# Performance work log

Measured on AMD Instinct MI355X. Metric: run time of the kernel, lower is better.

## Reference

```python
import jax, jax.numpy as jnp
import numpy as np

N, E, H, C, B = 20000, 320000, 4, 64, 64
D = H * C  # 256, output_dim_gnn
NEG_SLOPE = 0.2
EPS = 1e-5


def setup_inputs() -> dict:
    key = jax.random.key(0)
    ks = iter(jax.random.split(key, 40))
    s = 0.05
    inp = {}
    inp['x'] = jax.random.normal(next(ks), (N, 5), jnp.float32)
    inp['edge_index'] = jax.random.randint(next(ks), (2, E), 0, N, jnp.int64)
    inp['edge_attr'] = jax.random.normal(next(ks), (E, 63), jnp.float32)
    inp['batch'] = jnp.sort(jax.random.randint(next(ks), (N,), 0, B, jnp.int64))
    # node / edge embedding linears
    inp['node_W'] = jax.random.normal(next(ks), (5, D), jnp.float32) * s
    inp['node_b'] = jnp.zeros((D,), jnp.float32)
    inp['edge_W'] = jax.random.normal(next(ks), (63, D), jnp.float32) * s
    inp['edge_b'] = jnp.zeros((D,), jnp.float32)
    # two GATv2 layers + batch norms
    for i in range(2):
        inp[f'Wl{i}'] = jax.random.normal(next(ks), (D, H * C), jnp.float32) * s
        inp[f'bl{i}'] = jnp.zeros((H * C,), jnp.float32)
        inp[f'Wr{i}'] = jax.random.normal(next(ks), (D, H * C), jnp.float32) * s
        inp[f'br{i}'] = jnp.zeros((H * C,), jnp.float32)
        inp[f'We{i}'] = jax.random.normal(next(ks), (D, H * C), jnp.float32) * s
        inp[f'att{i}'] = jax.random.normal(next(ks), (H, C), jnp.float32) * s
        inp[f'bias{i}'] = jnp.zeros((H * C,), jnp.float32)
        inp[f'gamma{i}'] = jnp.ones((D,), jnp.float32)
        inp[f'beta{i}'] = jnp.zeros((D,), jnp.float32)
    # final MLP + output layer
    inp['mlp_W'] = jax.random.normal(next(ks), (D, C), jnp.float32) * s
    inp['mlp_b'] = jnp.zeros((C,), jnp.float32)
    inp['out_W'] = jax.random.normal(next(ks), (C, 5), jnp.float32) * s
    inp['out_b'] = jnp.zeros((5,), jnp.float32)
    return inp


def gatv2_conv(x, src, dst, e, Wl, bl, Wr, br, We, att, bias):
    # x: [N, D]; e: [E, D] (embedded edge features)
    xl = (x @ Wl + bl).reshape(N, H, C)  # source-side transform (lin_l)
    xr = (x @ Wr + br).reshape(N, H, C)  # target-side transform (lin_r)
    ee = (e @ We).reshape(E, H, C)       # lin_edge (no bias in PyG)
    m = xl[src] + xr[dst] + ee           # [E, H, C]
    alpha = jnp.einsum('ehc,hc->eh', jax.nn.leaky_relu(m, NEG_SLOPE), att)
    # segment softmax over incoming edges of each target node
    amax = jax.ops.segment_max(alpha, dst, num_segments=N)[dst]
    ex = jnp.exp(alpha - amax)
    denom = jax.ops.segment_sum(ex, dst, num_segments=N)[dst]
    a = ex / denom                        # [E, H]
    out = jax.ops.segment_sum(xl[src] * a[:, :, None], dst, num_segments=N)
    return out.reshape(N, H * C) + bias


def batch_norm(x, gamma, beta):
    mu = jnp.mean(x, axis=0)
    var = jnp.mean((x - mu) ** 2, axis=0)  # biased var (training-mode norm)
    return (x - mu) * jax.lax.rsqrt(var + EPS) * gamma + beta


def reference(x, edge_index, edge_attr, batch,
              node_W, node_b, edge_W, edge_b,
              Wl0, bl0, Wr0, br0, We0, att0, bias0, gamma0, beta0,
              Wl1, bl1, Wr1, br1, We1, att1, bias1, gamma1, beta1,
              mlp_W, mlp_b, out_W, out_b):
    src, dst = edge_index[0], edge_index[1]
    h = x @ node_W + node_b          # [N, D]
    e = edge_attr @ edge_W + edge_b  # [E, D]
    h = gatv2_conv(h, src, dst, e, Wl0, bl0, Wr0, br0, We0, att0, bias0)
    h = jax.nn.relu(batch_norm(h, gamma0, beta0))
    h = gatv2_conv(h, src, dst, e, Wl1, bl1, Wr1, br1, We1, att1, bias1)
    h = jax.nn.relu(batch_norm(h, gamma1, beta1))
    h = jax.nn.relu(h @ mlp_W + mlp_b)  # [N, C]
    # global mean pool per graph
    pooled = jax.ops.segment_sum(h, batch, num_segments=B)
    cnt = jax.ops.segment_sum(jnp.ones((N,), h.dtype), batch, num_segments=B)
    pooled = pooled / jnp.maximum(cnt, 1.0)[:, None]
    return pooled @ out_W + out_b  # [B, n_classes]
```

## Files before the change

### kernel.cpp

```cpp
#include <hip/hip_runtime.h>

#define NN 20000
#define EE 320000
#define BB 64

typedef _Float16 half8 __attribute__((ext_vector_type(8)));
typedef _Float16 half4 __attribute__((ext_vector_type(4)));
typedef float floatx4 __attribute__((ext_vector_type(4)));

__global__ void k_prep_edgeW(const float* __restrict__ edge_W, const float* __restrict__ edge_b,
                             const float* __restrict__ We0, const float* __restrict__ We1,
                             _Float16* __restrict__ Wpt0, _Float16* __restrict__ Wpt1) {
    __shared__ float row[256];
    int k = blockIdx.x, layer = blockIdx.y, j = threadIdx.x;
    row[j] = (k < 63) ? edge_W[k*256 + j] : edge_b[j];
    __syncthreads();
    const float* We = layer ? We1 : We0;
    float acc = 0.f;
    for (int t = 0; t < 256; ++t) acc += row[t] * We[t*256 + j];
    (layer ? Wpt1 : Wpt0)[j*64 + k] = (_Float16)acc;
}

__global__ void k_prep_acat(const float* __restrict__ node_W, const float* __restrict__ node_b,
                            const float* __restrict__ Wl0, const float* __restrict__ bl0,
                            const float* __restrict__ Wr0, const float* __restrict__ br0,
                            float* __restrict__ Acat) {
    __shared__ float row[256];
    int k = blockIdx.x, j = threadIdx.x;
    if (j < 256) row[j] = (k < 5) ? node_W[k*256 + j] : node_b[j];
    __syncthreads();
    int jj = j & 255;
    const float* W = (j < 256) ? Wl0 : Wr0;
    float acc = 0.f;
    for (int t = 0; t < 256; ++t) acc += row[t] * W[t*256 + jj];
    if (k == 5) acc += (j < 256) ? bl0[jj] : br0[jj];
    Acat[k*512 + j] = acc;
}

__global__ void k_prep_t16(const float* __restrict__ Wl1, const float* __restrict__ bl1,
                           const float* __restrict__ Wr1, const float* __restrict__ br1,
                           const float* __restrict__ mlp_W,
                           _Float16* __restrict__ WlWr1t, float* __restrict__ blr1,
                           _Float16* __restrict__ mlpWt) {
    int n = blockIdx.x, k = threadIdx.x;
    if (n < 512) {
        float v = (n < 256) ? Wl1[k*256 + n] : Wr1[k*256 + (n - 256)];
        WlWr1t[n*256 + k] = (_Float16)v;
        if (k == 0) blr1[n] = (n < 256) ? bl1[n] : br1[n - 256];
    } else {
        int nn = n - 512;
        mlpWt[nn*256 + k] = (_Float16)mlp_W[k*64 + nn];
    }
}

__global__ void k_hist(const int* __restrict__ ei, int* __restrict__ counts) {
    int e = blockIdx.x*256 + threadIdx.x;
    if (e < EE) atomicAdd(&counts[ei[EE + e]], 1);
}

__global__ __launch_bounds__(1024) void k_scan(const int* __restrict__ counts,
                                               int* __restrict__ row_ptr, int* __restrict__ cursor) {
    __shared__ int part[1024];
    int t = threadIdx.x;
    const int per = (NN + 1023) / 1024;
    int b0 = t*per, b1 = min(b0 + per, NN);
    int s = 0;
    for (int i = b0; i < b1; ++i) s += counts[i];
    part[t] = s; __syncthreads();
    for (int d = 1; d < 1024; d <<= 1) {
        int v = (t >= d) ? part[t-d] : 0;
        __syncthreads();
        part[t] += v;
        __syncthreads();
    }
    int run = (t == 0) ? 0 : part[t-1];
    for (int i = b0; i < b1; ++i) { row_ptr[i] = run; cursor[i] = run; run += counts[i]; }
    if (t == 0) row_ptr[NN] = EE;
}

__global__ void k_scatter(const int* __restrict__ ei, int* __restrict__ cursor,
                          int* __restrict__ pos, int* __restrict__ csr_src) {
    int e = blockIdx.x*256 + threadIdx.x;
    if (e < EE) {
        int d = ei[EE + e];
        int p = atomicAdd(&cursor[d], 1);
        pos[e] = p;
        csr_src[p] = ei[e];
    }
}

__global__ void k_permattr(const float* __restrict__ attr, const int* __restrict__ pos,
                           _Float16* __restrict__ attr16) {
    int tid = threadIdx.x;
    int w = tid >> 6, lane = tid & 63;
    int e = blockIdx.x*4 + w;
    if (e >= EE) return;
    float v = (lane < 63) ? attr[(size_t)e*63 + lane] : 1.0f;
    attr16[(size_t)pos[e]*64 + lane] = (_Float16)v;
}

__global__ void k_xlxr0(const float* __restrict__ x, const float* __restrict__ Acat,
                        _Float16* __restrict__ xlxr16) {
    int n = blockIdx.x, j = threadIdx.x;
    float a0 = Acat[5*512 + j], a1 = Acat[5*512 + 256 + j];
#pragma unroll
    for (int k = 0; k < 5; ++k) {
        float xv = x[n*5 + k];
        a0 += xv * Acat[k*512 + j];
        a1 += xv * Acat[k*512 + 256 + j];
    }
    xlxr16[(size_t)n*512 + j] = (_Float16)a0;
    xlxr16[(size_t)n*512 + 256 + j] = (_Float16)a1;
}

#define NPB 4
__global__ __launch_bounds__(256) void k_fused(const _Float16* __restrict__ attr16,
        const int* __restrict__ csrc, const int* __restrict__ row_ptr,
        const _Float16* __restrict__ Wpt, const float* __restrict__ att,
        const _Float16* __restrict__ xlxr16, const float* __restrict__ bias,
        float* __restrict__ gat) {
    int tid = threadIdx.x;
    int wave = tid >> 6, lane = tid & 63;
    int l15 = lane & 15, l4 = lane >> 4;
    int col = wave*64 + lane;

    __shared__ __align__(16) _Float16 xls[16][256];

    half8 bf[4][2];
    float attv[4];
#pragma unroll
    for (int ct = 0; ct < 4; ++ct) {
        int c = wave*64 + ct*16 + l15;
        attv[ct] = att[c];
        bf[ct][0] = *(const half8*)&Wpt[(size_t)c*64 + l4*8];
        bf[ct][1] = *(const half8*)&Wpt[(size_t)c*64 + 32 + l4*8];
    }
    float bv = bias[col];

    for (int i = 0; i < NPB; ++i) {
        int n = blockIdx.x*NPB + i;
        if (n >= NN) break;
        int s = row_ptr[n], e = row_ptr[n+1];
        if (e <= s) { gat[(size_t)n*256 + col] = bv; continue; }

        float xrf[4];
#pragma unroll
        for (int ct = 0; ct < 4; ++ct)
            xrf[ct] = (float)xlxr16[(size_t)n*512 + 256 + wave*64 + ct*16 + l15];

        float m_run = -3.0e38f, l_run = 0.f, out_acc = 0.f;
        for (int t0 = s; t0 < e; t0 += 16) {
            int nt = min(16, e - t0);
            {
                int r = tid >> 4, c0 = (tid & 15) * 16;
                int er = t0 + ((r < nt) ? r : 0);
                const _Float16* src = &xlxr16[(size_t)csrc[er]*512 + c0];
                *(half8*)&xls[r][c0]     = *(const half8*)&src[0];
                *(half8*)&xls[r][c0 + 8] = *(const half8*)&src[8];
            }
            __syncthreads();
            size_t ar = (size_t)(t0 + ((l15 < nt) ? l15 : 0)) * 64;
            half8 a0 = *(const half8*)&attr16[ar + l4*8];
            half8 a1 = *(const half8*)&attr16[ar + 32 + l4*8];
            floatx4 acc[4];
#pragma unroll
            for (int ct = 0; ct < 4; ++ct) {
                floatx4 z = {};
                acc[ct] = __builtin_amdgcn_mfma_f32_16x16x32_f16(a0, bf[ct][0], z, 0, 0, 0);
                acc[ct] = __builtin_amdgcn_mfma_f32_16x16x32_f16(a1, bf[ct][1], acc[ct], 0, 0, 0);
            }
            float p[4];
#pragma unroll
            for (int r = 0; r < 4; ++r) {
                int eidx = l4*4 + r;
                float pv = 0.f;
#pragma unroll
                for (int ct = 0; ct < 4; ++ct) {
                    float m = acc[ct][r] + (float)xls[eidx][wave*64 + ct*16 + l15] + xrf[ct];
                    float lr = (m > 0.f) ? m : 0.2f*m;
                    pv += lr * attv[ct];
                }
                pv += __shfl_xor(pv, 1);
                pv += __shfl_xor(pv, 2);
                pv += __shfl_xor(pv, 4);
                pv += __shfl_xor(pv, 8);
                p[r] = (eidx < nt) ? pv : -3.0e38f;
            }
            float aall[16];
#pragma unroll
            for (int k = 0; k < 16; ++k)
                aall[k] = __shfl(p[k & 3], (k >> 2) << 4);
            float mt = aall[0];
#pragma unroll
            for (int k = 1; k < 16; ++k) mt = fmaxf(mt, aall[k]);
            float mnew = fmaxf(m_run, mt);
            float scale = __expf(m_run - mnew);
            out_acc *= scale; l_run *= scale;
#pragma unroll
            for (int k = 0; k < 16; ++k) {
                float wk = __expf(aall[k] - mnew);
                l_run += wk;
                out_acc += wk * (float)xls[k][col];
            }
            m_run = mnew;
            __syncthreads();
        }
        gat[(size_t)n*256 + col] = out_acc / l_run + bv;
    }
}

__global__ void k_bn_stats(const float* __restrict__ X, float* __restrict__ stats) {
    int j = threadIdx.x;
    int shard = blockIdx.x & 15;
    float s = 0.f, q = 0.f;
    for (int r = blockIdx.x; r < NN; r += gridDim.x) {
        float v = X[(size_t)r*256 + j];
        s += v; q += v*v;
    }
    atomicAdd(&stats[shard*512 + j], s);
    atomicAdd(&stats[shard*512 + 256 + j], q);
}

__global__ void k_bn_final(const float* __restrict__ stats, const float* __restrict__ gamma,
                           const float* __restrict__ beta, float* __restrict__ ss) {
    int j = threadIdx.x;
    float s = 0.f, q = 0.f;
#pragma unroll
    for (int sh = 0; sh < 16; ++sh) {
        s += stats[sh*512 + j];
        q += stats[sh*512 + 256 + j];
    }
    float mean = s * (1.0f/NN);
    float var  = q * (1.0f/NN) - mean*mean;
    float sc = rsqrtf(var + 1e-5f) * gamma[j];
    ss[j] = sc;
    ss[256 + j] = beta[j] - mean*sc;
}

__global__ void k_bn_apply(const float* __restrict__ X, const float* __restrict__ ss,
                           _Float16* __restrict__ Hh) {
    size_t i4 = (size_t)blockIdx.x*256 + threadIdx.x;
    int col = (int)((i4*4) & 255);
    float4 v = *(const float4*)&X[i4*4];
    float4 sc = *(const float4*)&ss[col];
    float4 sh = *(const float4*)&ss[256 + col];
    half4 o;
    o[0] = (_Float16)fmaxf(v.x*sc.x + sh.x, 0.f);
    o[1] = (_Float16)fmaxf(v.y*sc.y + sh.y, 0.f);
    o[2] = (_Float16)fmaxf(v.z*sc.z + sh.z, 0.f);
    o[3] = (_Float16)fmaxf(v.w*sc.w + sh.w, 0.f);
    *(half4*)&Hh[i4*4] = o;
}

template<bool RELU, typename OT>
__global__ __launch_bounds__(256) void k_gemm(const _Float16* __restrict__ A, const _Float16* __restrict__ Bt,
                       const float* __restrict__ bias, OT* __restrict__ C,
                       int M, int K, int ldc) {
    __shared__ __align__(16) _Float16 As[128][72];
    __shared__ __align__(16) _Float16 Bs[64][72];
    int tid = threadIdx.x;
    int wave = tid >> 6, lane = tid & 63;
    int l15 = lane & 15, l4 = lane >> 4;
    int row0 = blockIdx.x*128, n0 = blockIdx.y*64;
    floatx4 acc[2][4] = {};
    for (int k0 = 0; k0 < K; k0 += 64) {
#pragma unroll
        for (int q = 0; q < 4; ++q) {
            int c = tid + q*256;
            int r = c >> 3, kc = (c & 7)*8;
            int gr = row0 + r; if (gr >= M) gr = M - 1;
            *(half8*)&As[r][kc] = *(const half8*)&A[(size_t)gr*K + k0 + kc];
        }
#pragma unroll
        for (int q = 0; q < 2; ++q) {
            int c = tid + q*256;
            int r = c >> 3, kc = (c & 7)*8;
            *(half8*)&Bs[r][kc] = *(const half8*)&Bt[(size_t)(n0 + r)*K + k0 + kc];
        }
        __syncthreads();
#pragma unroll
        for (int ks = 0; ks < 64; ks += 32) {
            half8 a0 = *(const half8*)&As[wave*32 + l15][ks + l4*8];
            half8 a1 = *(const half8*)&As[wave*32 + 16 + l15][ks + l4*8];
#pragma unroll
            for (int nb = 0; nb < 4; ++nb) {
                half8 b = *(const half8*)&Bs[nb*16 + l15][ks + l4*8];
                acc[0][nb] = __builtin_amdgcn_mfma_f32_16x16x32_f16(a0, b, acc[0][nb], 0, 0, 0);
                acc[1][nb] = __builtin_amdgcn_mfma_f32_16x16x32_f16(a1, b, acc[1][nb], 0, 0, 0);
            }
        }
        __syncthreads();
    }
#pragma unroll
    for (int m = 0; m < 2; ++m)
#pragma unroll
    for (int nb = 0; nb < 4; ++nb) {
        int col = n0 + nb*16 + l15;
        float bv = bias[col];
#pragma unroll
        for (int r = 0; r < 4; ++r) {
            int grow = row0 + wave*32 + m*16 + l4*4 + r;
            if (grow < M) {
                float v = acc[m][nb][r] + bv;
                if (RELU) v = fmaxf(v, 0.f);
                C[(size_t)grow*ldc + col] = (OT)v;
            }
        }
    }
}

__global__ void k_pool2(const float* __restrict__ mo, const int* __restrict__ batch,
                        float* __restrict__ pooledDiv) {
    int b = blockIdx.x;
    int j = threadIdx.x & 63, rg = threadIdx.x >> 6;
    int lo = 0, hi = NN;
    while (lo < hi) { int mid = (lo + hi) >> 1; if (batch[mid] < b) lo = mid + 1; else hi = mid; }
    int s = lo;
    lo = 0; hi = NN;
    while (lo < hi) { int mid = (lo + hi) >> 1; if (batch[mid] < b + 1) lo = mid + 1; else hi = mid; }
    int e = lo;
    float acc = 0.f;
    for (int r = s + rg; r < e; r += 4) acc += mo[(size_t)r*64 + j];
    __shared__ float red[256];
    red[threadIdx.x] = acc;
    __syncthreads();
    if (rg == 0) {
        float v = red[j] + red[64 + j] + red[128 + j] + red[192 + j];
        pooledDiv[b*64 + j] = v / fmaxf((float)(e - s), 1.f);
    }
}

__global__ void k_final(const float* __restrict__ pooledDiv,
                        const float* __restrict__ outW, const float* __restrict__ outb,
                        float* __restrict__ out) {
    int t = threadIdx.x;
    if (t >= 320) return;
    int b = t / 5, c = t % 5;
    float acc = outb[c];
    for (int k = 0; k < 64; ++k) acc += pooledDiv[b*64 + k] * outW[k*5 + c];
    out[t] = acc;
}

extern "C" void kernel_launch(void* const* d_in, const int* in_sizes, int n_in,
                              void* d_out, int out_size, void* d_ws, size_t ws_size,
                              hipStream_t stream) {
    const float* x      = (const float*)d_in[0];
    const int*   ei     = (const int*)d_in[1];
    const float* attr   = (const float*)d_in[2];
    const int*   batch  = (const int*)d_in[3];
    const float* node_W = (const float*)d_in[4];
    const float* node_b = (const float*)d_in[5];
    const float* edge_W = (const float*)d_in[6];
    const float* edge_b = (const float*)d_in[7];
    const float* Wl[2]   = {(const float*)d_in[8],  (const float*)d_in[17]};
    const float* bl[2]   = {(const float*)d_in[9],  (const float*)d_in[18]};
    const float* Wr[2]   = {(const float*)d_in[10], (const float*)d_in[19]};
    const float* br[2]   = {(const float*)d_in[11], (const float*)d_in[20]};
    const float* We[2]   = {(const float*)d_in[12], (const float*)d_in[21]};
    const float* att[2]  = {(const float*)d_in[13], (const float*)d_in[22]};
    const float* bias[2] = {(const float*)d_in[14], (const float*)d_in[23]};
    const float* gamma[2]= {(const float*)d_in[15], (const float*)d_in[24]};
    const float* beta[2] = {(const float*)d_in[16], (const float*)d_in[25]};
    const float* mlp_W = (const float*)d_in[26];
    const float* mlp_b = (const float*)d_in[27];
    const float* out_W = (const float*)d_in[28];
    const float* out_b = (const float*)d_in[29];
    float* out = (float*)d_out;

    char* p = (char*)d_ws;
    size_t off = 0;
    auto carve = [&](size_t bytes) -> void* {
        void* r = p + off;
        off = (off + bytes + 255) & ~(size_t)255;
        return r;
    };
    _Float16* Wpt0   = (_Float16*)carve(256*64*2);
    _Float16* Wpt1   = (_Float16*)carve(256*64*2);
    float*    Acat   = (float*)carve(6*512*4);
    _Float16* WlWr1t = (_Float16*)carve(512*256*2);
    float*    blr1   = (float*)carve(512*4);
    _Float16* mlpWt  = (_Float16*)carve(64*256*2);
    float*    ss     = (float*)carve(512*4);
    _Float16* xlxr16 = (_Float16*)carve((size_t)NN*512*2);
    float*    gat    = (float*)carve((size_t)NN*256*4);
    _Float16* h16    = (_Float16*)carve((size_t)NN*256*2);
    float*    mlo    = (float*)carve((size_t)NN*64*4);
    _Float16* attr16 = (_Float16*)carve((size_t)EE*64*2);
    int*      row_ptr= (int*)carve((NN+1)*4);
    int*      pos    = (int*)carve((size_t)EE*4);
    int*      csrc   = (int*)carve((size_t)EE*4);
    int*      cursor = (int*)carve(NN*4);
    float*    pooledDiv = (float*)carve(BB*64*4);
    char*     zz     = (char*)carve((NN + 16384)*4);
    int*      counts = (int*)zz;
    float*    stats  = (float*)(zz + (size_t)NN*4);
    if (off > ws_size) return;

    hipMemsetAsync(zz, 0, (size_t)(NN + 16384)*4, stream);
    k_prep_edgeW<<<dim3(64,2), 256, 0, stream>>>(edge_W, edge_b, We[0], We[1], Wpt0, Wpt1);
    k_prep_acat<<<6, 512, 0, stream>>>(node_W, node_b, Wl[0], bl[0], Wr[0], br[0], Acat);
    k_prep_t16<<<576, 256, 0, stream>>>(Wl[1], bl[1], Wr[1], br[1], mlp_W, WlWr1t, blr1, mlpWt);
    k_hist<<<(EE+255)/256, 256, 0, stream>>>(ei, counts);
    k_scan<<<1, 1024, 0, stream>>>(counts, row_ptr, cursor);
    k_scatter<<<(EE+255)/256, 256, 0, stream>>>(ei, cursor, pos, csrc);
    k_permattr<<<EE/4, 256, 0, stream>>>(attr, pos, attr16);
    k_xlxr0<<<NN, 256, 0, stream>>>(x, Acat, xlxr16);

    for (int L = 0; L < 2; ++L) {
        k_fused<<<(NN + NPB - 1)/NPB, 256, 0, stream>>>(attr16, csrc, row_ptr,
                 L ? Wpt1 : Wpt0, att[L], xlxr16, bias[L], gat);
        k_bn_stats<<<1024, 256, 0, stream>>>(gat, stats + L*8192);
        k_bn_final<<<1, 256, 0, stream>>>(stats + L*8192, gamma[L], beta[L], ss);
        k_bn_apply<<<NN*256/4/256, 256, 0, stream>>>(gat, ss, h16);
        if (L == 0)
            k_gemm<false, _Float16><<<dim3(157, 8), 256, 0, stream>>>(h16, WlWr1t, blr1, xlxr16, NN, 256, 512);
        else
            k_gemm<true, float><<<dim3(157, 1), 256, 0, stream>>>(h16, mlpWt, mlp_b, mlo, NN, 256, 64);
    }
    k_pool2<<<BB, 256, 0, stream>>>(mlo, batch, pooledDiv);
    k_final<<<1, 320, 0, stream>>>(pooledDiv, out_W, out_b, out);
}
```

Measured before the change: 459.2 us.

## Restructure GAT aggregation as per-wave pipelined stream and fuse BN apply into GEMM

The fused GAT kernel now processes the block's nodes as one continuous edge stream, with each wave owning its own 64-column slice. It double-buffers the gathered source rows in per-wave LDS and prefetches the next tile into registers, which removes the block-wide __syncthreads. The GAT output is stored as fp16 and the bias add is dropped, since training-mode batch norm cancels a per-column constant. The separate BN-apply kernel is removed and the scale/shift plus ReLU are folded into the GEMM's A-tile load. This cuts memory traffic and one launch, at the cost of fp16 precision for the pre-BN activations and more complex control flow.

```diff
diff --git a/kernel.cpp b/kernel.cpp
--- a/kernel.cpp
+++ b/kernel.cpp
@@ -5,7 +5,6 @@
 #define BB 64
 
 typedef _Float16 half8 __attribute__((ext_vector_type(8)));
-typedef _Float16 half4 __attribute__((ext_vector_type(4)));
 typedef float floatx4 __attribute__((ext_vector_type(4)));
 
 __global__ void k_prep_edgeW(const float* __restrict__ edge_W, const float* __restrict__ edge_b,
@@ -117,14 +116,12 @@
 __global__ __launch_bounds__(256) void k_fused(const _Float16* __restrict__ attr16,
         const int* __restrict__ csrc, const int* __restrict__ row_ptr,
         const _Float16* __restrict__ Wpt, const float* __restrict__ att,
-        const _Float16* __restrict__ xlxr16, const float* __restrict__ bias,
-        float* __restrict__ gat) {
+        const _Float16* __restrict__ xlxr16, _Float16* __restrict__ gat16) {
     int tid = threadIdx.x;
     int wave = tid >> 6, lane = tid & 63;
     int l15 = lane & 15, l4 = lane >> 4;
-    int col = wave*64 + lane;
-
-    __shared__ __align__(16) _Float16 xls[16][256];
+
+    __shared__ __align__(16) _Float16 xls[4][2][16][72];
 
     half8 bf[4][2];
     float attv[4];
@@ -135,86 +132,140 @@
         bf[ct][0] = *(const half8*)&Wpt[(size_t)c*64 + l4*8];
         bf[ct][1] = *(const half8*)&Wpt[(size_t)c*64 + 32 + l4*8];
     }
-    float bv = bias[col];
-
-    for (int i = 0; i < NPB; ++i) {
-        int n = blockIdx.x*NPB + i;
-        if (n >= NN) break;
-        int s = row_ptr[n], e = row_ptr[n+1];
-        if (e <= s) { gat[(size_t)n*256 + col] = bv; continue; }
-
-        float xrf[4];
-#pragma unroll
-        for (int ct = 0; ct < 4; ++ct)
-            xrf[ct] = (float)xlxr16[(size_t)n*512 + 256 + wave*64 + ct*16 + l15];
-
-        float m_run = -3.0e38f, l_run = 0.f, out_acc = 0.f;
-        for (int t0 = s; t0 < e; t0 += 16) {
-            int nt = min(16, e - t0);
-            {
-                int r = tid >> 4, c0 = (tid & 15) * 16;
-                int er = t0 + ((r < nt) ? r : 0);
-                const _Float16* src = &xlxr16[(size_t)csrc[er]*512 + c0];
-                *(half8*)&xls[r][c0]     = *(const half8*)&src[0];
-                *(half8*)&xls[r][c0 + 8] = *(const half8*)&src[8];
+
+    int n = blockIdx.x*NPB;
+    int nEnd = n + NPB; if (nEnd > NN) nEnd = NN;
+    int s_n = row_ptr[n];
+    int e_n;
+    for (;;) {
+        if (n >= nEnd) return;
+        e_n = row_ptr[n+1];
+        if (e_n > s_n) break;
+        gat16[(size_t)n*256 + wave*64 + lane] = (_Float16)0.f;
+        ++n; s_n = e_n;
+    }
+    const int E = row_ptr[nEnd];
+    int t0 = s_n;
+
+    half8 rx0, rx1, ra0, ra1, rb0, rb1;
+    int srow = lane >> 2, scol = (lane & 3) * 16;
+
+    {
+        int er = t0 + srow; if (er >= EE) er = EE - 1;
+        const _Float16* sp = &xlxr16[(size_t)csrc[er]*512 + wave*64 + scol];
+        rx0 = *(const half8*)&sp[0];
+        rx1 = *(const half8*)&sp[8];
+        int arow = t0 + l15; if (arow >= EE) arow = EE - 1;
+        const _Float16* ap = &attr16[(size_t)arow*64];
+        ra0 = *(const half8*)&ap[l4*8];
+        ra1 = *(const half8*)&ap[32 + l4*8];
+    }
+    *(half8*)&xls[wave][0][srow][scol]     = rx0;
+    *(half8*)&xls[wave][0][srow][scol + 8] = rx1;
+    int tn = (t0 + 16 < e_n) ? t0 + 16 : e_n;
+    bool hasNext = tn < E;
+    if (hasNext) {
+        int er = tn + srow; if (er >= EE) er = EE - 1;
+        const _Float16* sp = &xlxr16[(size_t)csrc[er]*512 + wave*64 + scol];
+        rx0 = *(const half8*)&sp[0];
+        rx1 = *(const half8*)&sp[8];
+        int arow = tn + l15; if (arow >= EE) arow = EE - 1;
+        const _Float16* ap = &attr16[(size_t)arow*64];
+        rb0 = *(const half8*)&ap[l4*8];
+        rb1 = *(const half8*)&ap[32 + l4*8];
+    }
+
+    float xrf[4];
+#pragma unroll
+    for (int ct = 0; ct < 4; ++ct)
+        xrf[ct] = (float)xlxr16[(size_t)n*512 + 256 + wave*64 + ct*16 + l15];
+
+    float m_run = -3.0e38f, l_run = 0.f, out_acc = 0.f;
+    int cur = 0;
+    for (;;) {
+        int nt = e_n - t0; if (nt > 16) nt = 16;
+        floatx4 acc[4];
+#pragma unroll
+        for (int ct = 0; ct < 4; ++ct) {
+            floatx4 z = {};
+            acc[ct] = __builtin_amdgcn_mfma_f32_16x16x32_f16(ra0, bf[ct][0], z, 0, 0, 0);
+            acc[ct] = __builtin_amdgcn_mfma_f32_16x16x32_f16(ra1, bf[ct][1], acc[ct], 0, 0, 0);
+        }
+        float p[4];
+#pragma unroll
+        for (int r = 0; r < 4; ++r) {
+            int eidx = l4*4 + r;
+            float pv = 0.f;
+#pragma unroll
+            for (int ct = 0; ct < 4; ++ct) {
+                float m = acc[ct][r] + (float)xls[wave][cur][eidx][ct*16 + l15] + xrf[ct];
+                float lr = (m > 0.f) ? m : 0.2f*m;
+                pv += lr * attv[ct];
             }
-            __syncthreads();
-            size_t ar = (size_t)(t0 + ((l15 < nt) ? l15 : 0)) * 64;
-            half8 a0 = *(const half8*)&attr16[ar + l4*8];
-            half8 a1 = *(const half8*)&attr16[ar + 32 + l4*8];
-            floatx4 acc[4];
-#pragma unroll
-            for (int ct = 0; ct < 4; ++ct) {
-                floatx4 z = {};
-                acc[ct] = __builtin_amdgcn_mfma_f32_16x16x32_f16(a0, bf[ct][0], z, 0, 0, 0);
-                acc[ct] = __builtin_amdgcn_mfma_f32_16x16x32_f16(a1, bf[ct][1], acc[ct], 0, 0, 0);
+            pv += __shfl_xor(pv, 1);
+            pv += __shfl_xor(pv, 2);
+            pv += __shfl_xor(pv, 4);
+            pv += __shfl_xor(pv, 8);
+            p[r] = (eidx < nt) ? pv : -3.0e38f;
+        }
+        float aall[16];
+#pragma unroll
+        for (int k = 0; k < 16; ++k)
+            aall[k] = __shfl(p[k & 3], (k >> 2) << 4);
+        float mt = aall[0];
+#pragma unroll
+        for (int k = 1; k < 16; ++k) mt = fmaxf(mt, aall[k]);
+        float mnew = fmaxf(m_run, mt);
+        float scale = __expf(m_run - mnew);
+        out_acc *= scale; l_run *= scale;
+#pragma unroll
+        for (int k = 0; k < 16; ++k) {
+            float wk = __expf(aall[k] - mnew);
+            l_run += wk;
+            out_acc += wk * (float)xls[wave][cur][k][lane];
+        }
+        m_run = mnew;
+        if (t0 + 16 >= e_n) {
+            gat16[(size_t)n*256 + wave*64 + lane] = (_Float16)(out_acc / l_run);
+            ++n; s_n = e_n;
+            for (;;) {
+                if (n >= nEnd) return;
+                e_n = row_ptr[n+1];
+                if (e_n > s_n) break;
+                gat16[(size_t)n*256 + wave*64 + lane] = (_Float16)0.f;
+                ++n; s_n = e_n;
             }
-            float p[4];
-#pragma unroll
-            for (int r = 0; r < 4; ++r) {
-                int eidx = l4*4 + r;
-                float pv = 0.f;
-#pragma unroll
-                for (int ct = 0; ct < 4; ++ct) {
-                    float m = acc[ct][r] + (float)xls[eidx][wave*64 + ct*16 + l15] + xrf[ct];
-                    float lr = (m > 0.f) ? m : 0.2f*m;
-                    pv += lr * attv[ct];
-                }
-                pv += __shfl_xor(pv, 1);
-                pv += __shfl_xor(pv, 2);
-                pv += __shfl_xor(pv, 4);
-                pv += __shfl_xor(pv, 8);
-                p[r] = (eidx < nt) ? pv : -3.0e38f;
-            }
-            float aall[16];
-#pragma unroll
-            for (int k = 0; k < 16; ++k)
-                aall[k] = __shfl(p[k & 3], (k >> 2) << 4);
-            float mt = aall[0];
-#pragma unroll
-            for (int k = 1; k < 16; ++k) mt = fmaxf(mt, aall[k]);
-            float mnew = fmaxf(m_run, mt);
-            float scale = __expf(m_run - mnew);
-            out_acc *= scale; l_run *= scale;
-#pragma unroll
-            for (int k = 0; k < 16; ++k) {
-                float wk = __expf(aall[k] - mnew);
-                l_run += wk;
-                out_acc += wk * (float)xls[k][col];
-            }
-            m_run = mnew;
-            __syncthreads();
-        }
-        gat[(size_t)n*256 + col] = out_acc / l_run + bv;
-    }
-}
-
-__global__ void k_bn_stats(const float* __restrict__ X, float* __restrict__ stats) {
+            m_run = -3.0e38f; l_run = 0.f; out_acc = 0.f;
+#pragma unroll
+            for (int ct = 0; ct < 4; ++ct)
+                xrf[ct] = (float)xlxr16[(size_t)n*512 + 256 + wave*64 + ct*16 + l15];
+        }
+        t0 = tn;
+        *(half8*)&xls[wave][cur^1][srow][scol]     = rx0;
+        *(half8*)&xls[wave][cur^1][srow][scol + 8] = rx1;
+        ra0 = rb0; ra1 = rb1;
+        tn = (t0 + 16 < e_n) ? t0 + 16 : e_n;
+        hasNext = tn < E;
+        if (hasNext) {
+            int er = tn + srow; if (er >= EE) er = EE - 1;
+            const _Float16* sp = &xlxr16[(size_t)csrc[er]*512 + wave*64 + scol];
+            rx0 = *(const half8*)&sp[0];
+            rx1 = *(const half8*)&sp[8];
+            int arow = tn + l15; if (arow >= EE) arow = EE - 1;
+            const _Float16* ap = &attr16[(size_t)arow*64];
+            rb0 = *(const half8*)&ap[l4*8];
+            rb1 = *(const half8*)&ap[32 + l4*8];
+        }
+        cur ^= 1;
+    }
+}
+
+__global__ void k_bn_stats(const _Float16* __restrict__ X, float* __restrict__ stats) {
     int j = threadIdx.x;
     int shard = blockIdx.x & 15;
     float s = 0.f, q = 0.f;
     for (int r = blockIdx.x; r < NN; r += gridDim.x) {
-        float v = X[(size_t)r*256 + j];
+        float v = (float)X[(size_t)r*256 + j];
         s += v; q += v*v;
     }
     atomicAdd(&stats[shard*512 + j], s);
@@ -237,25 +288,12 @@
     ss[256 + j] = beta[j] - mean*sc;
 }
 
-__global__ void k_bn_apply(const float* __restrict__ X, const float* __restrict__ ss,
-                           _Float16* __restrict__ Hh) {
-    size_t i4 = (size_t)blockIdx.x*256 + threadIdx.x;
-    int col = (int)((i4*4) & 255);
-    float4 v = *(const float4*)&X[i4*4];
-    float4 sc = *(const float4*)&ss[col];
-    float4 sh = *(const float4*)&ss[256 + col];
-    half4 o;
-    o[0] = (_Float16)fmaxf(v.x*sc.x + sh.x, 0.f);
-    o[1] = (_Float16)fmaxf(v.y*sc.y + sh.y, 0.f);
-    o[2] = (_Float16)fmaxf(v.z*sc.z + sh.z, 0.f);
-    o[3] = (_Float16)fmaxf(v.w*sc.w + sh.w, 0.f);
-    *(half4*)&Hh[i4*4] = o;
-}
-
 template<bool RELU, typename OT>
-__global__ __launch_bounds__(256) void k_gemm(const _Float16* __restrict__ A, const _Float16* __restrict__ Bt,
+__global__ __launch_bounds__(256) void k_gemm(const _Float16* __restrict__ A,
+                       const float* __restrict__ ssv,
+                       const _Float16* __restrict__ Bt,
                        const float* __restrict__ bias, OT* __restrict__ C,
-                       int M, int K, int ldc) {
+                       int M, int ldc) {
     __shared__ __align__(16) _Float16 As[128][72];
     __shared__ __align__(16) _Float16 Bs[64][72];
     int tid = threadIdx.x;
@@ -263,19 +301,27 @@
     int l15 = lane & 15, l4 = lane >> 4;
     int row0 = blockIdx.x*128, n0 = blockIdx.y*64;
     floatx4 acc[2][4] = {};
-    for (int k0 = 0; k0 < K; k0 += 64) {
+    for (int k0 = 0; k0 < 256; k0 += 64) {
 #pragma unroll
         for (int q = 0; q < 4; ++q) {
             int c = tid + q*256;
             int r = c >> 3, kc = (c & 7)*8;
             int gr = row0 + r; if (gr >= M) gr = M - 1;
-            *(half8*)&As[r][kc] = *(const half8*)&A[(size_t)gr*K + k0 + kc];
+            half8 g = *(const half8*)&A[(size_t)gr*256 + k0 + kc];
+            _Float16 tmp[8];
+#pragma unroll
+            for (int i = 0; i < 8; ++i) {
+                int colk = k0 + kc + i;
+                float v = (float)g[i]*ssv[colk] + ssv[256 + colk];
+                tmp[i] = (_Float16)fmaxf(v, 0.f);
+            }
+            *(half8*)&As[r][kc] = *(half8*)tmp;
         }
 #pragma unroll
         for (int q = 0; q < 2; ++q) {
             int c = tid + q*256;
             int r = c >> 3, kc = (c & 7)*8;
-            *(half8*)&Bs[r][kc] = *(const half8*)&Bt[(size_t)(n0 + r)*K + k0 + kc];
+            *(half8*)&Bs[r][kc] = *(const half8*)&Bt[(size_t)(n0 + r)*256 + k0 + kc];
         }
         __syncthreads();
 #pragma unroll
@@ -358,7 +404,6 @@
     const float* br[2]   = {(const float*)d_in[11], (const float*)d_in[20]};
     const float* We[2]   = {(const float*)d_in[12], (const float*)d_in[21]};
     const float* att[2]  = {(const float*)d_in[13], (const float*)d_in[22]};
-    const float* bias[2] = {(const float*)d_in[14], (const float*)d_in[23]};
     const float* gamma[2]= {(const float*)d_in[15], (const float*)d_in[24]};
     const float* beta[2] = {(const float*)d_in[16], (const float*)d_in[25]};
     const float* mlp_W = (const float*)d_in[26];
@@ -382,8 +427,7 @@
     _Float16* mlpWt  = (_Float16*)carve(64*256*2);
     float*    ss     = (float*)carve(512*4);
     _Float16* xlxr16 = (_Float16*)carve((size_t)NN*512*2);
-    float*    gat    = (float*)carve((size_t)NN*256*4);
-    _Float16* h16    = (_Float16*)carve((size_t)NN*256*2);
+    _Float16* gat16  = (_Float16*)carve((size_t)NN*256*2);
     float*    mlo    = (float*)carve((size_t)NN*64*4);
     _Float16* attr16 = (_Float16*)carve((size_t)EE*64*2);
     int*      row_ptr= (int*)carve((NN+1)*4);
@@ -408,14 +452,13 @@
 
     for (int L = 0; L < 2; ++L) {
         k_fused<<<(NN + NPB - 1)/NPB, 256, 0, stream>>>(attr16, csrc, row_ptr,
-                 L ? Wpt1 : Wpt0, att[L], xlxr16, bias[L], gat);
-        k_bn_stats<<<1024, 256, 0, stream>>>(gat, stats + L*8192);
+                 L ? Wpt1 : Wpt0, att[L], xlxr16, gat16);
+        k_bn_stats<<<1024, 256, 0, stream>>>(gat16, stats + L*8192);
         k_bn_final<<<1, 256, 0, stream>>>(stats + L*8192, gamma[L], beta[L], ss);
-        k_bn_apply<<<NN*256/4/256, 256, 0, stream>>>(gat, ss, h16);
         if (L == 0)
-            k_gemm<false, _Float16><<<dim3(157, 8), 256, 0, stream>>>(h16, WlWr1t, blr1, xlxr16, NN, 256, 512);
+            k_gemm<false, _Float16><<<dim3(157, 8), 256, 0, stream>>>(gat16, ss, WlWr1t, blr1, xlxr16, NN, 512);
         else
-            k_gemm<true, float><<<dim3(157, 1), 256, 0, stream>>>(h16, mlpWt, mlp_b, mlo, NN, 256, 64);
+            k_gemm<true, float><<<dim3(157, 1), 256, 0, stream>>>(gat16, ss, mlpWt, mlp_b, mlo, NN, 64);
     }
     k_pool2<<<BB, 256, 0, stream>>>(mlo, batch, pooledDiv);
     k_final<<<1, 320, 0, stream>>>(pooledDiv, out_W, out_b, out);
```

Measured after the change: 466.1 us. Within noise of the previous version (+1.5%).
